# Kernel optimization log

Measured on AMD Instinct MI355X. Metric: run time of the kernel, lower is better.

## Reference

```python
import jax, jax.numpy as jnp
import numpy as np

D_MODEL = 1024
NUM_HEADS = 16
D_K = D_MODEL // NUM_HEADS


def setup_inputs() -> dict:
    key = jax.random.key(0)
    ks = jax.random.split(key, 5)
    x = jax.random.normal(ks[0], (8, 1024, D_MODEL), dtype=jnp.float32)
    s_in = 1.0 / np.sqrt(D_MODEL)
    W_qkv = jax.random.normal(ks[1], (D_MODEL, 3 * D_MODEL), dtype=jnp.float32) * s_in
    b_qkv = jax.random.normal(ks[2], (3 * D_MODEL,), dtype=jnp.float32) * 0.01
    W_o = jax.random.normal(ks[3], (D_MODEL, D_MODEL), dtype=jnp.float32) * s_in
    b_o = jax.random.normal(ks[4], (D_MODEL,), dtype=jnp.float32) * 0.01
    return {"x": x, "W_qkv": W_qkv, "b_qkv": b_qkv, "W_o": W_o, "b_o": b_o}


def reference(x, W_qkv, b_qkv, W_o, b_o):
    B, N, D = x.shape
    qkv = x @ W_qkv + b_qkv                      # [B, N, 3D]
    qkv = qkv.reshape(B, N, 3, NUM_HEADS, D_K)
    qkv = jnp.transpose(qkv, (2, 0, 3, 1, 4))    # [3, B, H, N, d_k]
    q, k, v = qkv[0], qkv[1], qkv[2]
    scale = 1.0 / np.sqrt(D_K).astype(np.float32)
    attn = jnp.einsum('bhqd,bhkd->bhqk', q, k) * scale
    attn = jax.nn.softmax(attn, axis=-1)
    out = jnp.einsum('bhqk,bhkd->bhqd', attn, v)  # [B, H, N, d_k]
    out = jnp.transpose(out, (0, 2, 1, 3)).reshape(B, N, D)
    return out @ W_o + b_o
```

## Files before the change

### kernel.cpp

```cpp
#include <hip/hip_runtime.h>


typedef __attribute__((ext_vector_type(8))) short bf16x8;
typedef __attribute__((ext_vector_type(4))) float f32x4;

#define GLOAD_LDS16(gp, lp)                                                              \
  __builtin_amdgcn_global_load_lds((const __attribute__((address_space(1))) void*)(gp),  \
                                   (__attribute__((address_space(3))) void*)(lp), 16, 0, 0)

__device__ __forceinline__ unsigned short f2bf(float f) {
  unsigned int u = __float_as_uint(f);
  u += 0x7fffu + ((u >> 16) & 1u);
  return (unsigned short)(u >> 16);
}

__global__ __launch_bounds__(256) void cast_f32_to_bf16(
    const float* __restrict__ in, unsigned short* __restrict__ out, int n4) {
  int stride = gridDim.x * blockDim.x;
  for (int i = blockIdx.x * blockDim.x + threadIdx.x; i < n4; i += stride) {
    float4 v = reinterpret_cast<const float4*>(in)[i];
    ushort4 o;
    o.x = f2bf(v.x); o.y = f2bf(v.y); o.z = f2bf(v.z); o.w = f2bf(v.w);
    reinterpret_cast<ushort4*>(out)[i] = o;
  }
}

__global__ __launch_bounds__(256) void transpose_cast(
    const float* __restrict__ W, unsigned short* __restrict__ Wt, int R, int C) {
  __shared__ float tile[32][33];
  int tx = threadIdx.x & 31, ty = threadIdx.x >> 5;
  int c0 = blockIdx.x * 32, r0 = blockIdx.y * 32;
  #pragma unroll
  for (int i = 0; i < 4; i++) {
    int r = r0 + ty + i * 8;
    tile[ty + i * 8][tx] = W[(size_t)r * C + c0 + tx];
  }
  __syncthreads();
  #pragma unroll
  for (int i = 0; i < 4; i++) {
    int c = c0 + ty + i * 8;
    Wt[(size_t)c * R + r0 + tx] = f2bf(tile[tx][ty + i * 8]);
  }
}

template <int MODE>
__global__ __launch_bounds__(512) void gemm256(
    const unsigned short* __restrict__ A, const unsigned short* __restrict__ Bt,
    const float* __restrict__ bias, unsigned short* __restrict__ qkv_out,
    float* __restrict__ Cout) {
  __shared__ __align__(16) unsigned short As[2][128 * 64];
  __shared__ __align__(16) unsigned short Bs[2][256 * 64];
  const int t = threadIdx.x;
  const int lane = t & 63, wid = t >> 6;
  const int lr = lane & 15, g = lane >> 4;
  const int wm = wid >> 2, wn = wid & 3;

  const int nwg = gridDim.x * gridDim.y;
  const int id = blockIdx.x + gridDim.x * blockIdx.y;
  const int sw = (id & 7) * (nwg >> 3) + (id >> 3);
  const int bx = sw % gridDim.x, by = sw / gridDim.x;
  const int row0 = by * 128, col0 = bx * 256;

  const int srow = t >> 3, sch = t & 7;

  auto stA = [&](int buf, int kt, int j) {
    int row = j * 64 + srow;
    int ch = sch ^ (row & 7);
    GLOAD_LDS16(A + (size_t)(row0 + row) * 1024 + kt * 64 + ch * 8,
                (char*)&As[buf][0] + j * 8192 + t * 16);
  };
  auto stB = [&](int buf, int kt, int j) {
    int row = j * 64 + srow;
    int ch = sch ^ (row & 7);
    GLOAD_LDS16(Bt + (size_t)(col0 + row) * 1024 + kt * 64 + ch * 8,
                (char*)&Bs[buf][0] + j * 8192 + t * 16);
  };
  auto rdA = [&](int buf, int c, int m) -> bf16x8 {
    int r = wm * 64 + m * 16 + lr;
    return *(const bf16x8*)((const char*)&As[buf][0] + r * 128 +
                            ((c * 64 + g * 16) ^ ((r & 7) << 4)));
  };
  auto rdB = [&](int buf, int c, int n) -> bf16x8 {
    int r = wn * 64 + n * 16 + lr;
    return *(const bf16x8*)((const char*)&Bs[buf][0] + r * 128 +
                            ((c * 64 + g * 16) ^ ((r & 7) << 4)));
  };

  f32x4 acc[4][4] = {};

  stA(0, 0, 0); stA(0, 0, 1);
  stB(0, 0, 0); stB(0, 0, 1); stB(0, 0, 2); stB(0, 0, 3);
  asm volatile("s_waitcnt vmcnt(0)" ::: "memory");
  __builtin_amdgcn_s_barrier();

  for (int kt = 0; kt < 16; kt++) {
    const int buf = kt & 1;
    const bool pf = (kt + 1 < 16);
    if (kt > 0) {
      if (pf) {
        stA(buf ^ 1, kt + 1, 0); stA(buf ^ 1, kt + 1, 1);
        asm volatile("s_waitcnt vmcnt(2)" ::: "memory");
      } else {
        asm volatile("s_waitcnt vmcnt(0)" ::: "memory");
      }
      __builtin_amdgcn_s_barrier();
    } else if (pf) {
      stA(buf ^ 1, kt + 1, 0); stA(buf ^ 1, kt + 1, 1);
    }

    bf16x8 a0[4], b0[4];
    #pragma unroll
    for (int m = 0; m < 4; m++) a0[m] = rdA(buf, 0, m);
    #pragma unroll
    for (int n = 0; n < 4; n++) b0[n] = rdB(buf, 0, n);
    if (pf) { stB(buf ^ 1, kt + 1, 0); stB(buf ^ 1, kt + 1, 1); }
    __builtin_amdgcn_s_barrier();
    asm volatile("s_waitcnt lgkmcnt(0)" ::: "memory");
    __builtin_amdgcn_sched_barrier(0);
    __builtin_amdgcn_s_setprio(1);
    #pragma unroll
    for (int m = 0; m < 4; m++)
      #pragma unroll
      for (int n = 0; n < 4; n++)
        acc[m][n] = __builtin_amdgcn_mfma_f32_16x16x32_bf16(a0[m], b0[n], acc[m][n], 0, 0, 0);
    __builtin_amdgcn_s_setprio(0);
    __builtin_amdgcn_s_barrier();

    bf16x8 a1[4], b1[4];
    #pragma unroll
    for (int m = 0; m < 4; m++) a1[m] = rdA(buf, 1, m);
    #pragma unroll
    for (int n = 0; n < 4; n++) b1[n] = rdB(buf, 1, n);
    if (pf) { stB(buf ^ 1, kt + 1, 2); stB(buf ^ 1, kt + 1, 3); }
    __builtin_amdgcn_s_barrier();
    asm volatile("s_waitcnt lgkmcnt(0)" ::: "memory");
    __builtin_amdgcn_sched_barrier(0);
    __builtin_amdgcn_s_setprio(1);
    #pragma unroll
    for (int m = 0; m < 4; m++)
      #pragma unroll
      for (int n = 0; n < 4; n++)
        acc[m][n] = __builtin_amdgcn_mfma_f32_16x16x32_bf16(a1[m], b1[n], acc[m][n], 0, 0, 0);
    __builtin_amdgcn_s_setprio(0);
    __builtin_amdgcn_s_barrier();
  }

  if (MODE == 0) {
    const int which = col0 >> 10;
    if (which == 2) {
      #pragma unroll
      for (int m = 0; m < 4; m++) {
        int row = row0 + wm * 64 + m * 16 + g * 4;
        int bb = row >> 10, nn = row & 1023;
        #pragma unroll
        for (int n = 0; n < 4; n++) {
          int col = col0 + wn * 64 + n * 16 + lr;
          int cc = col & 1023;
          int h = cc >> 6, dk = cc & 63;
          float bv = bias[col];
          ushort4 w;
          w.x = f2bf(acc[m][n][0] + bv);
          w.y = f2bf(acc[m][n][1] + bv);
          w.z = f2bf(acc[m][n][2] + bv);
          w.w = f2bf(acc[m][n][3] + bv);
          size_t idx = ((size_t)2 << 23) + (((size_t)(bb * 16 + h)) << 16) +
                       (size_t)dk * 1024 + nn;
          *(ushort4*)(qkv_out + idx) = w;
        }
      }
    } else {
      #pragma unroll
      for (int m = 0; m < 4; m++) {
        #pragma unroll
        for (int n = 0; n < 4; n++) {
          int col = col0 + wn * 64 + n * 16 + lr;
          int cc = col & 1023;
          int h = cc >> 6, dk = cc & 63;
          #pragma unroll
          for (int r = 0; r < 4; r++) {
            int row = row0 + wm * 64 + m * 16 + g * 4 + r;
            int bb = row >> 10, nn = row & 1023;
            float v = acc[m][n][r] + bias[col];
            if (which == 0) v *= 0.125f;
            size_t idx = ((size_t)which << 23) +
                         (((size_t)((bb * 16 + h) * 1024 + nn)) << 6) + dk;
            qkv_out[idx] = f2bf(v);
          }
        }
      }
    }
  } else {
    #pragma unroll
    for (int m = 0; m < 4; m++) {
      #pragma unroll
      for (int n = 0; n < 4; n++) {
        int col = col0 + wn * 64 + n * 16 + lr;
        #pragma unroll
        for (int r = 0; r < 4; r++) {
          int row = row0 + wm * 64 + m * 16 + g * 4 + r;
          Cout[(size_t)row * 1024 + col] = acc[m][n][r] + bias[col];
        }
      }
    }
  }
}

__global__ __launch_bounds__(512) void attn_mfma(
    const unsigned short* __restrict__ qkv, unsigned short* __restrict__ attn_out) {
  __shared__ __align__(16) unsigned short K_lds[2][64 * 64];
  __shared__ __align__(16) unsigned short V_lds[2][64 * 64];
  __shared__ __align__(16) unsigned short P_lds[128 * 64];

  const int bid = ((blockIdx.x & 7) << 7) + (blockIdx.x >> 3);
  const int bh = bid >> 3, qt = bid & 7;
  const unsigned short* Qp = qkv + ((size_t)bh << 16);
  const unsigned short* Kp = qkv + (1u << 23) + ((size_t)bh << 16);
  const unsigned short* Vt = qkv + (2u << 23) + ((size_t)bh << 16);

  const int t = threadIdx.x;
  const int lane = t & 63, wid = t >> 6;
  const int lr = lane & 15, g = lane >> 4;

  bf16x8 qf[2];
  {
    int qrow = qt * 128 + wid * 16 + lr;
    qf[0] = *(const bf16x8*)(Qp + (size_t)qrow * 64 + g * 8);
    qf[1] = *(const bf16x8*)(Qp + (size_t)qrow * 64 + 32 + g * 8);
  }

  const int srow = t >> 3;
  const int sch  = (t & 7) ^ (srow & 7);
  const int so   = t * 16;

  auto stage = [&](int buf, int kt) {
    GLOAD_LDS16(Kp + (size_t)(kt * 64 + srow) * 64 + sch * 8, (char*)&K_lds[buf][0] + so);
    GLOAD_LDS16(Vt + (size_t)srow * 1024 + kt * 64 + sch * 8, (char*)&V_lds[buf][0] + so);
  };

  f32x4 o_acc[4] = {};
  float den[4] = {0.f, 0.f, 0.f, 0.f};

  stage(0, 0);
  __syncthreads();
  int buf = 0;
  for (int kt = 0; kt < 16; kt++) {
    if (kt + 1 < 16) stage(buf ^ 1, kt + 1);

    f32x4 s4[4] = {};
    __builtin_amdgcn_s_setprio(1);
    #pragma unroll
    for (int ks = 0; ks < 4; ks++) {
      int krow = ks * 16 + lr;
      #pragma unroll
      for (int c = 0; c < 2; c++) {
        bf16x8 kf = *(const bf16x8*)((char*)&K_lds[buf][0] + krow * 128 +
                                     ((c * 64 + g * 16) ^ ((krow & 7) << 4)));
        s4[ks] = __builtin_amdgcn_mfma_f32_16x16x32_bf16(qf[c], kf, s4[ks], 0, 0, 0);
      }
    }
    __builtin_amdgcn_s_setprio(0);

    #pragma unroll
    for (int ks = 0; ks < 4; ks++) {
      #pragma unroll
      for (int r = 0; r < 4; r++) {
        float e = __expf(s4[ks][r]);
        den[r] += e;
        int q = wid * 16 + g * 4 + r;
        *(unsigned short*)((char*)P_lds + q * 128 +
                           (((ks * 16 + lr) * 2) ^ ((q & 7) << 4))) = f2bf(e);
      }
    }

    bf16x8 pa[2];
    {
      int q = wid * 16 + lr;
      #pragma unroll
      for (int c = 0; c < 2; c++)
        pa[c] = *(const bf16x8*)((char*)P_lds + q * 128 +
                                 ((c * 64 + g * 16) ^ ((q & 7) << 4)));
    }
    __builtin_amdgcn_s_setprio(1);
    #pragma unroll
    for (int ds_ = 0; ds_ < 4; ds_++) {
      int drow = ds_ * 16 + lr;
      #pragma unroll
      for (int c = 0; c < 2; c++) {
        bf16x8 vf = *(const bf16x8*)((char*)&V_lds[buf][0] + drow * 128 +
                                     ((c * 64 + g * 16) ^ ((drow & 7) << 4)));
        o_acc[ds_] = __builtin_amdgcn_mfma_f32_16x16x32_bf16(pa[c], vf, o_acc[ds_], 0, 0, 0);
      }
    }
    __builtin_amdgcn_s_setprio(0);
    __syncthreads();
    buf ^= 1;
  }

  #pragma unroll
  for (int r = 0; r < 4; r++) {
    den[r] += __shfl_xor(den[r], 1, 64);
    den[r] += __shfl_xor(den[r], 2, 64);
    den[r] += __shfl_xor(den[r], 4, 64);
    den[r] += __shfl_xor(den[r], 8, 64);
  }

  const int bb = bh >> 4, h = bh & 15;
  #pragma unroll
  for (int ds_ = 0; ds_ < 4; ds_++) {
    #pragma unroll
    for (int r = 0; r < 4; r++) {
      int q = qt * 128 + wid * 16 + g * 4 + r;
      int d = h * 64 + ds_ * 16 + lr;
      attn_out[((size_t)(bb * 1024 + q)) * 1024 + d] = f2bf(o_acc[ds_][r] / den[r]);
    }
  }
}

extern "C" void kernel_launch(void* const* d_in, const int* in_sizes, int n_in,
                              void* d_out, int out_size, void* d_ws, size_t ws_size,
                              hipStream_t stream) {
  const float* x     = (const float*)d_in[0];
  const float* W_qkv = (const float*)d_in[1];
  const float* b_qkv = (const float*)d_in[2];
  const float* W_o   = (const float*)d_in[3];
  const float* b_o   = (const float*)d_in[4];
  float* out = (float*)d_out;

  unsigned short* ws      = (unsigned short*)d_ws;
  unsigned short* x_bf    = ws;
  unsigned short* wqkv_t  = x_bf + 8388608;
  unsigned short* wo_t    = wqkv_t + 3145728;
  unsigned short* qkv     = wo_t + 1048576;
  unsigned short* attn_o  = qkv + 25165824;

  cast_f32_to_bf16<<<2048, 256, 0, stream>>>(x, x_bf, 8388608 / 4);
  transpose_cast<<<dim3(96, 32), 256, 0, stream>>>(W_qkv, wqkv_t, 1024, 3072);
  transpose_cast<<<dim3(32, 32), 256, 0, stream>>>(W_o, wo_t, 1024, 1024);

  gemm256<0><<<dim3(12, 64), 512, 0, stream>>>(x_bf, wqkv_t, b_qkv, qkv, nullptr);
  attn_mfma<<<1024, 512, 0, stream>>>(qkv, attn_o);
  gemm256<1><<<dim3(4, 64), 512, 0, stream>>>(attn_o, wo_t, b_o, nullptr, out);
}
```

Before: 184.2 us.

## Rework GEMM into 4-stage K32 pipeline with per-mode tile shapes

Replaces the double-buffered K=64 GEMM with a 4-buffer K=32 pipeline that prefetches three stages ahead, using counted vmcnt waits and a new 4-chunk XOR swizzle. The QKV projection now uses 256x192 tiles (512 blocks) while the output projection keeps 128x256, and launch bounds request 2 blocks per CU. The aim is to hide global load latency better and balance the grid across CUs. It adds register pressure from larger accumulator tiles and relies on exact vmcnt counts matching the number of issued loads per stage.

```diff
diff --git a/kernel.cpp b/kernel.cpp
--- a/kernel.cpp
+++ b/kernel.cpp
@@ -44,12 +44,20 @@
 }
 
 template <int MODE>
-__global__ __launch_bounds__(512) void gemm256(
-    const unsigned short* __restrict__ A, const unsigned short* __restrict__ Bt,
+__global__ __launch_bounds__(512, 2) void gemm_dp(
+    const unsigned short* __restrict__ Aop, const unsigned short* __restrict__ Bop,
     const float* __restrict__ bias, unsigned short* __restrict__ qkv_out,
     float* __restrict__ Cout) {
-  __shared__ __align__(16) unsigned short As[2][128 * 64];
-  __shared__ __align__(16) unsigned short Bs[2][256 * 64];
+  constexpr int BM = (MODE == 0) ? 256 : 128;
+  constexpr int BN = (MODE == 0) ? 192 : 256;
+  constexpr int MF = BM / 32;
+  constexpr int NF = BN / 64;
+  constexpr int WNSZ = BN / 4;
+  constexpr int NA = BM / 128;
+
+  __shared__ __align__(16) unsigned short As[4][BM * 32];
+  __shared__ __align__(16) unsigned short Bs[4][BN * 32];
+
   const int t = threadIdx.x;
   const int lane = t & 63, wid = t >> 6;
   const int lr = lane & 15, g = lane >> 4;
@@ -59,105 +67,105 @@
   const int id = blockIdx.x + gridDim.x * blockIdx.y;
   const int sw = (id & 7) * (nwg >> 3) + (id >> 3);
   const int bx = sw % gridDim.x, by = sw / gridDim.x;
-  const int row0 = by * 128, col0 = bx * 256;
-
-  const int srow = t >> 3, sch = t & 7;
-
-  auto stA = [&](int buf, int kt, int j) {
-    int row = j * 64 + srow;
-    int ch = sch ^ (row & 7);
-    GLOAD_LDS16(A + (size_t)(row0 + row) * 1024 + kt * 64 + ch * 8,
-                (char*)&As[buf][0] + j * 8192 + t * 16);
-  };
-  auto stB = [&](int buf, int kt, int j) {
-    int row = j * 64 + srow;
-    int ch = sch ^ (row & 7);
-    GLOAD_LDS16(Bt + (size_t)(col0 + row) * 1024 + kt * 64 + ch * 8,
-                (char*)&Bs[buf][0] + j * 8192 + t * 16);
-  };
-  auto rdA = [&](int buf, int c, int m) -> bf16x8 {
-    int r = wm * 64 + m * 16 + lr;
-    return *(const bf16x8*)((const char*)&As[buf][0] + r * 128 +
-                            ((c * 64 + g * 16) ^ ((r & 7) << 4)));
-  };
-  auto rdB = [&](int buf, int c, int n) -> bf16x8 {
-    int r = wn * 64 + n * 16 + lr;
-    return *(const bf16x8*)((const char*)&Bs[buf][0] + r * 128 +
-                            ((c * 64 + g * 16) ^ ((r & 7) << 4)));
-  };
-
-  f32x4 acc[4][4] = {};
-
-  stA(0, 0, 0); stA(0, 0, 1);
-  stB(0, 0, 0); stB(0, 0, 1); stB(0, 0, 2); stB(0, 0, 3);
-  asm volatile("s_waitcnt vmcnt(0)" ::: "memory");
-  __builtin_amdgcn_s_barrier();
-
-  for (int kt = 0; kt < 16; kt++) {
-    const int buf = kt & 1;
-    const bool pf = (kt + 1 < 16);
-    if (kt > 0) {
-      if (pf) {
-        stA(buf ^ 1, kt + 1, 0); stA(buf ^ 1, kt + 1, 1);
-        asm volatile("s_waitcnt vmcnt(2)" ::: "memory");
-      } else {
-        asm volatile("s_waitcnt vmcnt(0)" ::: "memory");
-      }
-      __builtin_amdgcn_s_barrier();
-    } else if (pf) {
-      stA(buf ^ 1, kt + 1, 0); stA(buf ^ 1, kt + 1, 1);
-    }
-
-    bf16x8 a0[4], b0[4];
-    #pragma unroll
-    for (int m = 0; m < 4; m++) a0[m] = rdA(buf, 0, m);
-    #pragma unroll
-    for (int n = 0; n < 4; n++) b0[n] = rdB(buf, 0, n);
-    if (pf) { stB(buf ^ 1, kt + 1, 0); stB(buf ^ 1, kt + 1, 1); }
+  const int row0 = by * BM, col0 = bx * BN;
+
+  const int srow = t >> 2;
+  const int sch  = (t & 3) ^ ((srow >> 1) & 3);
+
+  auto stageA = [&](int buf, int kt2) {
+    #pragma unroll
+    for (int j = 0; j < NA; j++) {
+      GLOAD_LDS16(Aop + (size_t)(row0 + j * 128 + srow) * 1024 + kt2 * 32 + sch * 8,
+                  (char*)&As[buf][0] + j * 8192 + t * 16);
+    }
+  };
+  auto stageB = [&](int buf, int kt2) {
+    #pragma unroll
+    for (int j = 0; j < 2; j++) {
+      int rb = (MODE == 0) ? j * 64 : j * 128;
+      GLOAD_LDS16(Bop + (size_t)(col0 + rb + srow) * 1024 + kt2 * 32 + sch * 8,
+                  (char*)&Bs[buf][0] + rb * 64 + t * 16);
+    }
+  };
+  auto rdA = [&](int buf, int m) -> bf16x8 {
+    int r = wm * (BM / 2) + m * 16 + lr;
+    return *(const bf16x8*)((const char*)&As[buf][0] + r * 64 +
+                            ((g ^ ((r >> 1) & 3)) * 16));
+  };
+  auto rdB = [&](int buf, int n) -> bf16x8 {
+    int r = wn * WNSZ + n * 16 + lr;
+    return *(const bf16x8*)((const char*)&Bs[buf][0] + r * 64 +
+                            ((g ^ ((r >> 1) & 3)) * 16));
+  };
+
+  f32x4 acc[MF][NF] = {};
+
+  stageA(0, 0); stageB(0, 0);
+  stageA(1, 1); stageB(1, 1);
+  stageA(2, 2); stageB(2, 2);
+
+  for (int kt = 0; kt < 32; kt++) {
+    const int buf = kt & 3;
+    const int rem = 31 - kt;
+    if (rem >= 2) {
+      if constexpr (MODE == 0) asm volatile("s_waitcnt vmcnt(8)" ::: "memory");
+      else                     asm volatile("s_waitcnt vmcnt(6)" ::: "memory");
+    } else if (rem == 1) {
+      if constexpr (MODE == 0) asm volatile("s_waitcnt vmcnt(4)" ::: "memory");
+      else                     asm volatile("s_waitcnt vmcnt(3)" ::: "memory");
+    } else {
+      asm volatile("s_waitcnt vmcnt(0)" ::: "memory");
+    }
+    __builtin_amdgcn_s_barrier();
+
+    bf16x8 bfr[NF], afr[MF / 2];
+
+    #pragma unroll
+    for (int n = 0; n < NF; n++) bfr[n] = rdB(buf, n);
+    #pragma unroll
+    for (int m = 0; m < MF / 2; m++) afr[m] = rdA(buf, m);
+    if (kt <= 28) stageA((kt + 3) & 3, kt + 3);
     __builtin_amdgcn_s_barrier();
     asm volatile("s_waitcnt lgkmcnt(0)" ::: "memory");
     __builtin_amdgcn_sched_barrier(0);
     __builtin_amdgcn_s_setprio(1);
     #pragma unroll
-    for (int m = 0; m < 4; m++)
-      #pragma unroll
-      for (int n = 0; n < 4; n++)
-        acc[m][n] = __builtin_amdgcn_mfma_f32_16x16x32_bf16(a0[m], b0[n], acc[m][n], 0, 0, 0);
+    for (int m = 0; m < MF / 2; m++)
+      #pragma unroll
+      for (int n = 0; n < NF; n++)
+        acc[m][n] = __builtin_amdgcn_mfma_f32_16x16x32_bf16(afr[m], bfr[n], acc[m][n], 0, 0, 0);
     __builtin_amdgcn_s_setprio(0);
     __builtin_amdgcn_s_barrier();
 
-    bf16x8 a1[4], b1[4];
-    #pragma unroll
-    for (int m = 0; m < 4; m++) a1[m] = rdA(buf, 1, m);
-    #pragma unroll
-    for (int n = 0; n < 4; n++) b1[n] = rdB(buf, 1, n);
-    if (pf) { stB(buf ^ 1, kt + 1, 2); stB(buf ^ 1, kt + 1, 3); }
+    #pragma unroll
+    for (int m = 0; m < MF / 2; m++) afr[m] = rdA(buf, MF / 2 + m);
+    if (kt <= 28) stageB((kt + 3) & 3, kt + 3);
     __builtin_amdgcn_s_barrier();
     asm volatile("s_waitcnt lgkmcnt(0)" ::: "memory");
     __builtin_amdgcn_sched_barrier(0);
     __builtin_amdgcn_s_setprio(1);
     #pragma unroll
-    for (int m = 0; m < 4; m++)
-      #pragma unroll
-      for (int n = 0; n < 4; n++)
-        acc[m][n] = __builtin_amdgcn_mfma_f32_16x16x32_bf16(a1[m], b1[n], acc[m][n], 0, 0, 0);
+    for (int m = 0; m < MF / 2; m++)
+      #pragma unroll
+      for (int n = 0; n < NF; n++)
+        acc[MF / 2 + m][n] =
+            __builtin_amdgcn_mfma_f32_16x16x32_bf16(afr[m], bfr[n], acc[MF / 2 + m][n], 0, 0, 0);
     __builtin_amdgcn_s_setprio(0);
     __builtin_amdgcn_s_barrier();
   }
 
-  if (MODE == 0) {
-    const int which = col0 >> 10;
-    if (which == 2) {
-      #pragma unroll
-      for (int m = 0; m < 4; m++) {
-        int row = row0 + wm * 64 + m * 16 + g * 4;
-        int bb = row >> 10, nn = row & 1023;
-        #pragma unroll
-        for (int n = 0; n < 4; n++) {
-          int col = col0 + wn * 64 + n * 16 + lr;
-          int cc = col & 1023;
-          int h = cc >> 6, dk = cc & 63;
-          float bv = bias[col];
+  #pragma unroll
+  for (int m = 0; m < MF; m++) {
+    const int row = row0 + wm * (BM / 2) + m * 16 + g * 4;
+    #pragma unroll
+    for (int n = 0; n < NF; n++) {
+      const int col = col0 + wn * WNSZ + n * 16 + lr;
+      if constexpr (MODE == 0) {
+        const int which = col >> 10;
+        const int cc = col & 1023, h = cc >> 6, dk = cc & 63;
+        const int bb = row >> 10, nn = row & 1023;
+        const float bv = bias[col];
+        if (which == 2) {
           ushort4 w;
           w.x = f2bf(acc[m][n][0] + bv);
           w.y = f2bf(acc[m][n][1] + bv);
@@ -166,40 +174,20 @@
           size_t idx = ((size_t)2 << 23) + (((size_t)(bb * 16 + h)) << 16) +
                        (size_t)dk * 1024 + nn;
           *(ushort4*)(qkv_out + idx) = w;
-        }
-      }
-    } else {
-      #pragma unroll
-      for (int m = 0; m < 4; m++) {
-        #pragma unroll
-        for (int n = 0; n < 4; n++) {
-          int col = col0 + wn * 64 + n * 16 + lr;
-          int cc = col & 1023;
-          int h = cc >> 6, dk = cc & 63;
+        } else {
+          const float sc = (which == 0) ? 0.125f : 1.0f;
           #pragma unroll
           for (int r = 0; r < 4; r++) {
-            int row = row0 + wm * 64 + m * 16 + g * 4 + r;
-            int bb = row >> 10, nn = row & 1023;
-            float v = acc[m][n][r] + bias[col];
-            if (which == 0) v *= 0.125f;
             size_t idx = ((size_t)which << 23) +
-                         (((size_t)((bb * 16 + h) * 1024 + nn)) << 6) + dk;
-            qkv_out[idx] = f2bf(v);
+                         (((size_t)((bb * 16 + h) * 1024 + nn + r)) << 6) + dk;
+            qkv_out[idx] = f2bf((acc[m][n][r] + bv) * sc);
           }
         }
-      }
-    }
-  } else {
-    #pragma unroll
-    for (int m = 0; m < 4; m++) {
-      #pragma unroll
-      for (int n = 0; n < 4; n++) {
-        int col = col0 + wn * 64 + n * 16 + lr;
+      } else {
+        const float bv = bias[col];
         #pragma unroll
-        for (int r = 0; r < 4; r++) {
-          int row = row0 + wm * 64 + m * 16 + g * 4 + r;
-          Cout[(size_t)row * 1024 + col] = acc[m][n][r] + bias[col];
-        }
+        for (int r = 0; r < 4; r++)
+          Cout[(size_t)(row + r) * 1024 + col] = acc[m][n][r] + bv;
       }
     }
   }
@@ -337,7 +325,7 @@
   transpose_cast<<<dim3(96, 32), 256, 0, stream>>>(W_qkv, wqkv_t, 1024, 3072);
   transpose_cast<<<dim3(32, 32), 256, 0, stream>>>(W_o, wo_t, 1024, 1024);
 
-  gemm256<0><<<dim3(12, 64), 512, 0, stream>>>(x_bf, wqkv_t, b_qkv, qkv, nullptr);
+  gemm_dp<0><<<dim3(16, 32), 512, 0, stream>>>(x_bf, wqkv_t, b_qkv, qkv, nullptr);
   attn_mfma<<<1024, 512, 0, stream>>>(qkv, attn_o);
-  gemm256<1><<<dim3(4, 64), 512, 0, stream>>>(attn_o, wo_t, b_o, nullptr, out);
-}
+  gemm_dp<1><<<dim3(4, 64), 512, 0, stream>>>(attn_o, wo_t, b_o, nullptr, out);
+}
```

After: 170.7 us. 7.3% less time.
